# Optimization experiments

Hardware: AMD Instinct MI355X
Metric: run time of the kernel (lower is better)

The kernel has to match this reference:

```python
import jax, jax.numpy as jnp
import numpy as np

N_ENTITIES = 200000
N_USERS = 100000
DIM = 64
N_EDGES = 1000000
N_INTER = 1000000
N_REL = 33
N_INTERACTION_TYPES = 8


def segment_softmax(x, seg, num_segments):
    # two-pass numerically stable segment softmax (torch_scatter.scatter_softmax)
    m = jax.ops.segment_max(x, seg, num_segments=num_segments)
    e = jnp.exp(x - m[seg])
    s = jax.ops.segment_sum(e, seg, num_segments=num_segments)
    return e / s[seg]


def setup_inputs() -> dict:
    key = jax.random.key(0)
    ks = jax.random.split(key, 9)
    return {
        "entity_emb": jax.random.normal(ks[0], (N_ENTITIES, DIM), dtype=jnp.float32),
        "user_emb": jax.random.normal(ks[1], (N_USERS, DIM), dtype=jnp.float32),
        "interaction_emb": jax.random.normal(ks[2], (N_INTERACTION_TYPES, DIM), dtype=jnp.float32),
        "relation_emb": jax.random.normal(ks[3], (N_REL, DIM), dtype=jnp.float32),
        "edge_index": jax.random.randint(ks[4], (2, N_EDGES), 0, N_ENTITIES, dtype=jnp.int32),
        "edge_type": jax.random.randint(ks[5], (N_EDGES,), 1, N_REL, dtype=jnp.int32),
        "user_index": jax.random.randint(ks[6], (N_INTER,), 0, N_USERS, dtype=jnp.int32),
        "item_index": jax.random.randint(ks[7], (N_INTER,), 0, N_ENTITIES, dtype=jnp.int32),
        "interact_type": jax.random.randint(ks[8], (N_INTER,), 0, N_INTERACTION_TYPES, dtype=jnp.int32),
    }


def reference(entity_emb, user_emb, interaction_emb, relation_emb,
              edge_index, edge_type, user_index, item_index, interact_type):
    n_entities = entity_emb.shape[0]
    n_users = user_emb.shape[0]
    head, tail = edge_index[0], edge_index[1]

    # --- entity aggregation over KG edges ---
    neigh = entity_emb[tail]                                      # [E, D]
    w1 = jnp.sum(neigh * relation_emb[edge_type - 1], axis=1) / 8.0   # [E]
    w1 = segment_softmax(w1, head, n_entities)[:, None]           # [E, 1]
    entity_agg = jax.ops.segment_sum(neigh * w1, head, num_segments=n_entities)  # [n_entities, D]

    # --- user aggregation over interactions (agg_method='attention') ---
    interact_entity_emb = entity_emb[item_index]                  # [I, D]
    att = jnp.sum(interaction_emb[interact_type] * user_emb[user_index] * interact_entity_emb, axis=1)  # [I]
    att_w = segment_softmax(att, user_index, n_users)[:, None]    # [I, 1]
    user_agg = jax.ops.segment_sum(att_w * interact_entity_emb, user_index, num_segments=n_users)  # [n_users, D]

    return entity_agg, user_agg, att_w, w1
```

## Files before the change

### kernel.cpp

```cpp
#include <hip/hip_runtime.h>
#include <hip/hip_bf16.h>
#include <hip/hip_fp16.h>

#define DIM 64
#define RELS 32
#define SCAN_B 512
#define TILE_V 64

__device__ __forceinline__ unsigned int pk_h2(float a, float b) {
    __half2 h = __float22half2_rn(make_float2(a, b));
    return *reinterpret_cast<unsigned int*>(&h);
}
__device__ __forceinline__ float4 h4_to_f4(uint2 u) {
    __half2 h0 = *reinterpret_cast<__half2*>(&u.x);
    __half2 h1 = *reinterpret_cast<__half2*>(&u.y);
    float2 f0 = __half22float2(h0);
    float2 f1 = __half22float2(h1);
    return make_float4(f0.x, f0.y, f1.x, f1.y);
}

__global__ __launch_bounds__(256, 4) void buildM_deg(
    const float* __restrict__ ent, const float* __restrict__ rel,
    __hip_bfloat16* __restrict__ M, uint2* __restrict__ entH,
    const int* __restrict__ head, const int* __restrict__ uidx,
    unsigned int* __restrict__ degS,
    unsigned char* __restrict__ rank_e, unsigned char* __restrict__ rank_i,
    int nE, int E, int I, int gM, int Q, int NSEG) {
    __shared__ float4 entL[TILE_V * 17];
    __shared__ float relS[4][16][33];
    int tx = threadIdx.x;
    int bid = blockIdx.x;
    int g = bid / 7, slot = bid - g * 7;

    if (slot >= 2) {
        int t = (g * 5 + (slot - 2)) * 256 + tx;
        if (t < E + I) {
            int k = (t >= Q) + (t >= 2 * Q) + (t >= 3 * Q);
            unsigned int* dk = degS + (size_t)k * NSEG;
            if (t < E) {
                rank_e[t] = (unsigned char)atomicAdd(&dk[head[t]], 1u);
            } else {
                int e = t - E;
                rank_i[e] = (unsigned char)atomicAdd(&dk[nE + uidx[e]], 1u);
            }
        }
        return;
    }

    int mb = g * 2 + slot;
    if (mb >= gM) return;
    int vg = tx >> 4, rg = tx & 15;
    int base = mb * TILE_V;
    const float4* rel4 = (const float4*)rel;
    #pragma unroll
    for (int k = 0; k < 2; k++) {
        int idx = tx + k * 256;
        float4 v = rel4[idx];
        int r = idx >> 4, d4 = idx & 15;
        relS[0][d4][r] = v.x; relS[1][d4][r] = v.y;
        relS[2][d4][r] = v.z; relS[3][d4][r] = v.w;
    }
    const float4* ent4 = (const float4*)ent;
    #pragma unroll
    for (int k = 0; k < 4; k++) {
        int idx = tx + k * 256;
        int row = idx >> 4, col = idx & 15;
        int v = base + row;
        float4 val = make_float4(0.f, 0.f, 0.f, 0.f);
        if (v < nE) {
            val = ent4[(size_t)v * 16 + col];
            entH[(size_t)v * 16 + col] = make_uint2(pk_h2(val.x, val.y), pk_h2(val.z, val.w));
        }
        entL[row * 17 + col] = val;
    }
    __syncthreads();

    float acc[4][2] = {{0.f,0.f},{0.f,0.f},{0.f,0.f},{0.f,0.f}};
    int r0 = rg * 2;
    #pragma unroll 2
    for (int d4 = 0; d4 < 16; d4++) {
        float4 a0 = entL[(vg * 4 + 0) * 17 + d4];
        float4 a1 = entL[(vg * 4 + 1) * 17 + d4];
        float4 a2 = entL[(vg * 4 + 2) * 17 + d4];
        float4 a3 = entL[(vg * 4 + 3) * 17 + d4];
        float bx0 = relS[0][d4][r0],     by0 = relS[1][d4][r0];
        float bz0 = relS[2][d4][r0],     bw0 = relS[3][d4][r0];
        float bx1 = relS[0][d4][r0 + 1], by1 = relS[1][d4][r0 + 1];
        float bz1 = relS[2][d4][r0 + 1], bw1 = relS[3][d4][r0 + 1];
        acc[0][0] = fmaf(a0.x,bx0, fmaf(a0.y,by0, fmaf(a0.z,bz0, fmaf(a0.w,bw0, acc[0][0]))));
        acc[1][0] = fmaf(a1.x,bx0, fmaf(a1.y,by0, fmaf(a1.z,bz0, fmaf(a1.w,bw0, acc[1][0]))));
        acc[2][0] = fmaf(a2.x,bx0, fmaf(a2.y,by0, fmaf(a2.z,bz0, fmaf(a2.w,bw0, acc[2][0]))));
        acc[3][0] = fmaf(a3.x,bx0, fmaf(a3.y,by0, fmaf(a3.z,bz0, fmaf(a3.w,bw0, acc[3][0]))));
        acc[0][1] = fmaf(a0.x,bx1, fmaf(a0.y,by1, fmaf(a0.z,bz1, fmaf(a0.w,bw1, acc[0][1]))));
        acc[1][1] = fmaf(a1.x,bx1, fmaf(a1.y,by1, fmaf(a1.z,bz1, fmaf(a1.w,bw1, acc[1][1]))));
        acc[2][1] = fmaf(a2.x,bx1, fmaf(a2.y,by1, fmaf(a2.z,bz1, fmaf(a2.w,bw1, acc[2][1]))));
        acc[3][1] = fmaf(a3.x,bx1, fmaf(a3.y,by1, fmaf(a3.z,bz1, fmaf(a3.w,bw1, acc[3][1]))));
    }
    __hip_bfloat162* M2 = (__hip_bfloat162*)M;
    #pragma unroll
    for (int i = 0; i < 4; i++) {
        int v = base + vg * 4 + i;
        if (v < nE) {
            __hip_bfloat16 h0 = __float2bfloat16(acc[i][0] * 0.125f);
            __hip_bfloat16 h1 = __float2bfloat16(acc[i][1] * 0.125f);
            M2[(size_t)v * 16 + rg] = __halves2bfloat162(h0, h1);
        }
    }
}

__global__ __launch_bounds__(SCAN_B) void scan_partial(
    const unsigned int* __restrict__ degS, unsigned int* __restrict__ part, int n) {
    __shared__ unsigned int lds[SCAN_B];
    int i = blockIdx.x * SCAN_B + threadIdx.x;
    unsigned int v = 0;
    if (i < n) v = degS[i] + degS[n + i] + degS[2 * (size_t)n + i] + degS[3 * (size_t)n + i];
    lds[threadIdx.x] = v;
    __syncthreads();
    for (int off = SCAN_B >> 1; off > 0; off >>= 1) {
        if (threadIdx.x < off) lds[threadIdx.x] += lds[threadIdx.x + off];
        __syncthreads();
    }
    if (threadIdx.x == 0) part[blockIdx.x] = lds[0];
}

__global__ __launch_bounds__(1024) void scan_block(unsigned int* __restrict__ part, int nb) {
    __shared__ unsigned int lds[1024];
    int t = threadIdx.x;
    unsigned int v = (t < nb) ? part[t] : 0u;
    lds[t] = v;
    __syncthreads();
    for (int off = 1; off < 1024; off <<= 1) {
        unsigned int x = (t >= off) ? lds[t - off] : 0u;
        __syncthreads();
        lds[t] += x;
        __syncthreads();
    }
    if (t < nb) part[t] = lds[t] - v;
}

__global__ __launch_bounds__(SCAN_B) void scan_final(
    const unsigned int* __restrict__ degS, const unsigned int* __restrict__ part,
    unsigned int* __restrict__ offs0, unsigned int* __restrict__ offs123,
    int n, unsigned int total) {
    __shared__ unsigned int lds[SCAN_B];
    int t = threadIdx.x;
    int i = blockIdx.x * SCAN_B + t;
    unsigned int a0 = 0, a1 = 0, a2 = 0, a3 = 0, tot = 0;
    if (i < n) {
        a0 = degS[i]; a1 = degS[n + i];
        a2 = degS[2 * (size_t)n + i]; a3 = degS[3 * (size_t)n + i];
        tot = a0 + a1 + a2 + a3;
    }
    lds[t] = tot;
    __syncthreads();
    for (int off = 1; off < SCAN_B; off <<= 1) {
        unsigned int x = (t >= off) ? lds[t - off] : 0u;
        __syncthreads();
        lds[t] += x;
        __syncthreads();
    }
    if (i < n) {
        unsigned int base = part[blockIdx.x] + lds[t] - tot;
        offs0[i] = base;
        offs123[i] = base + a0;
        offs123[(size_t)n + i] = base + a0 + a1;
        offs123[2 * (size_t)n + i] = base + a0 + a1 + a2;
    }
    if (blockIdx.x == 0 && t == 0) offs0[n] = total;
}

__global__ __launch_bounds__(256) void scatter32(
    const __hip_bfloat16* __restrict__ M,
    const int* __restrict__ head, const int* __restrict__ tail, const int* __restrict__ etype,
    const int* __restrict__ uidx, const int* __restrict__ iidx, const int* __restrict__ ttype,
    const unsigned char* __restrict__ rank_e, const unsigned char* __restrict__ rank_i,
    const unsigned int* __restrict__ offs0, const unsigned int* __restrict__ offs123,
    unsigned long long* __restrict__ pay64, unsigned int* __restrict__ payu,
    float* __restrict__ e_sc, unsigned int* __restrict__ slotu,
    int E, int I, int nE, int Q, int NSEG) {
    int t = blockIdx.x * blockDim.x + threadIdx.x;
    if (t >= E + I) return;
    int k = (t >= Q) + (t >= 2 * Q) + (t >= 3 * Q);
    if (t < E) {
        int s = head[t];
        unsigned int base = (k == 0) ? offs0[s] : offs123[(size_t)(k - 1) * NSEG + s];
        int tl = tail[t];
        float sc = __bfloat162float(M[(size_t)tl * RELS + (etype[t] - 1)]);
        e_sc[t] = sc;
        unsigned int p = base + rank_e[t];
        unsigned long long v = ((unsigned long long)__float_as_uint(sc) << 32) | (unsigned int)tl;
        __builtin_nontemporal_store(v, &pay64[p]);
    } else {
        int e = t - E;
        int s = nE + uidx[e];
        unsigned int base = (k == 0) ? offs0[s] : offs123[(size_t)(k - 1) * NSEG + s];
        unsigned int p = base + rank_i[e] - (unsigned)E;
        unsigned int v = (unsigned int)iidx[e] | ((unsigned int)ttype[e] << 27);
        __builtin_nontemporal_store(v, &payu[p]);
        slotu[e] = p;
    }
}

__global__ __launch_bounds__(256) void fused_agg(
    const uint2* __restrict__ entH, const float* __restrict__ usr,
    const float* __restrict__ itc,
    const unsigned long long* __restrict__ pay64, const unsigned int* __restrict__ payu,
    const unsigned int* __restrict__ offs0,
    float* __restrict__ patt, float2* __restrict__ msum,
    float* __restrict__ aggE, float* __restrict__ aggU,
    int nE, int nU, int E, int gAE) {
    __shared__ float4 itcL[8][16];
    int tx = threadIdx.x;
    int bid = blockIdx.x;

    if (bid < gAE) {
        int t = bid * 256 + tx;
        int h = t >> 4, l = t & 15;
        if (h >= nE) return;
        unsigned int off = offs0[h];
        unsigned int d = offs0[h + 1] - off;
        float m = -3.0e38f, inv = 0.f;
        float4 acc = make_float4(0.f, 0.f, 0.f, 0.f);
        if (d) {
            float m0 = -3.0e38f, s0 = 0.f, m1 = -3.0e38f, s1 = 0.f;
            float4 A0 = make_float4(0.f,0.f,0.f,0.f), A1 = make_float4(0.f,0.f,0.f,0.f);
            unsigned long long v0 = pay64[off];
            uint2 b0 = entH[(size_t)(unsigned int)(v0 & 0xffffffffu) * 16 + l];
            unsigned long long v1 = 0; uint2 b1 = b0;
            if (d > 1) { v1 = pay64[off + 1]; b1 = entH[(size_t)(unsigned int)(v1 & 0xffffffffu) * 16 + l]; }
            for (unsigned int j = 0; j < d; j += 2) {
                unsigned long long nv0 = v0, nv1 = v1; uint2 nb0 = b0, nb1 = b1;
                if (j + 2 < d) { nv0 = pay64[off + j + 2]; nb0 = entH[(size_t)(unsigned int)(nv0 & 0xffffffffu) * 16 + l]; }
                if (j + 3 < d) { nv1 = pay64[off + j + 3]; nb1 = entH[(size_t)(unsigned int)(nv1 & 0xffffffffu) * 16 + l]; }
                {
                    float sc = __uint_as_float((unsigned int)(v0 >> 32));
                    float mn = fmaxf(m0, sc);
                    float sca = __expf(m0 - mn), w = __expf(sc - mn);
                    float4 a = h4_to_f4(b0);
                    s0 = s0 * sca + w;
                    A0.x = A0.x * sca + w * a.x; A0.y = A0.y * sca + w * a.y;
                    A0.z = A0.z * sca + w * a.z; A0.w = A0.w * sca + w * a.w;
                    m0 = mn;
                }
                if (j + 1 < d) {
                    float sc = __uint_as_float((unsigned int)(v1 >> 32));
                    float mn = fmaxf(m1, sc);
                    float sca = __expf(m1 - mn), w = __expf(sc - mn);
                    float4 a = h4_to_f4(b1);
                    s1 = s1 * sca + w;
                    A1.x = A1.x * sca + w * a.x; A1.y = A1.y * sca + w * a.y;
                    A1.z = A1.z * sca + w * a.z; A1.w = A1.w * sca + w * a.w;
                    m1 = mn;
                }
                v0 = nv0; b0 = nb0; v1 = nv1; b1 = nb1;
            }
            float mn = fmaxf(m0, m1);
            float e0 = __expf(m0 - mn), e1 = __expf(m1 - mn);
            float s = s0 * e0 + s1 * e1;
            inv = 1.f / s;
            acc.x = A0.x * e0 + A1.x * e1; acc.y = A0.y * e0 + A1.y * e1;
            acc.z = A0.z * e0 + A1.z * e1; acc.w = A0.w * e0 + A1.w * e1;
            m = mn;
        }
        if (l == 0) msum[h] = make_float2(m, inv);
        acc.x *= inv; acc.y *= inv; acc.z *= inv; acc.w *= inv;
        ((float4*)(aggE + (size_t)h * DIM))[l] = acc;
        return;
    }

    if (tx < 128) itcL[tx >> 4][tx & 15] = ((const float4*)itc)[tx];
    __syncthreads();
    int t = (bid - gAE) * 256 + tx;
    int h = t >> 4, l = t & 15;
    if (h >= nU) return;
    int hs = nE + h;
    unsigned int off = offs0[hs] - (unsigned)E;
    unsigned int d = offs0[hs + 1] - offs0[hs];
    float m = -3.0e38f, inv = 0.f;
    float4 acc = make_float4(0.f, 0.f, 0.f, 0.f);
    float4 ur = ((const float4*)(usr + (size_t)h * DIM))[l];
    if (d) {
        float m0 = -3.0e38f, s0 = 0.f, m1 = -3.0e38f, s1 = 0.f;
        float4 A0 = make_float4(0.f,0.f,0.f,0.f), A1 = make_float4(0.f,0.f,0.f,0.f);
        unsigned int v0 = payu[off];
        uint2 b0 = entH[(size_t)(v0 & 0x7ffffffu) * 16 + l];
        unsigned int v1 = 0; uint2 b1 = b0;
        if (d > 1) { v1 = payu[off + 1]; b1 = entH[(size_t)(v1 & 0x7ffffffu) * 16 + l]; }
        for (unsigned int j = 0; j < d; j += 2) {
            unsigned int nv0 = v0, nv1 = v1; uint2 nb0 = b0, nb1 = b1;
            if (j + 2 < d) { nv0 = payu[off + j + 2]; nb0 = entH[(size_t)(nv0 & 0x7ffffffu) * 16 + l]; }
            if (j + 3 < d) { nv1 = payu[off + j + 3]; nb1 = entH[(size_t)(nv1 & 0x7ffffffu) * 16 + l]; }
            {
                float4 a = h4_to_f4(b0);
                float4 c = itcL[v0 >> 27][l];
                float p = a.x * ur.x * c.x + a.y * ur.y * c.y
                        + a.z * ur.z * c.z + a.w * ur.w * c.w;
                p += __shfl_xor(p, 1);
                p += __shfl_xor(p, 2);
                p += __shfl_xor(p, 4);
                p += __shfl_xor(p, 8);
                if (l == 0) patt[off + j] = p;
                float mn = fmaxf(m0, p);
                float sca = __expf(m0 - mn), w = __expf(p - mn);
                s0 = s0 * sca + w;
                A0.x = A0.x * sca + w * a.x; A0.y = A0.y * sca + w * a.y;
                A0.z = A0.z * sca + w * a.z; A0.w = A0.w * sca + w * a.w;
                m0 = mn;
            }
            if (j + 1 < d) {
                float4 a = h4_to_f4(b1);
                float4 c = itcL[v1 >> 27][l];
                float p = a.x * ur.x * c.x + a.y * ur.y * c.y
                        + a.z * ur.z * c.z + a.w * ur.w * c.w;
                p += __shfl_xor(p, 1);
                p += __shfl_xor(p, 2);
                p += __shfl_xor(p, 4);
                p += __shfl_xor(p, 8);
                if (l == 0) patt[off + j + 1] = p;
                float mn = fmaxf(m1, p);
                float sca = __expf(m1 - mn), w = __expf(p - mn);
                s1 = s1 * sca + w;
                A1.x = A1.x * sca + w * a.x; A1.y = A1.y * sca + w * a.y;
                A1.z = A1.z * sca + w * a.z; A1.w = A1.w * sca + w * a.w;
                m1 = mn;
            }
            v0 = nv0; b0 = nb0; v1 = nv1; b1 = nb1;
        }
        float mn = fmaxf(m0, m1);
        float e0 = __expf(m0 - mn), e1 = __expf(m1 - mn);
        float s = s0 * e0 + s1 * e1;
        inv = 1.f / s;
        acc.x = A0.x * e0 + A1.x * e1; acc.y = A0.y * e0 + A1.y * e1;
        acc.z = A0.z * e0 + A1.z * e1; acc.w = A0.w * e0 + A1.w * e1;
        m = mn;
    }
    if (l == 0) msum[hs] = make_float2(m, inv);
    acc.x *= inv; acc.y *= inv; acc.z *= inv; acc.w *= inv;
    ((float4*)(aggU + (size_t)h * DIM))[l] = acc;
}

__global__ __launch_bounds__(256) void wout(
    const int* __restrict__ head, const int* __restrict__ uidx,
    const float* __restrict__ e_sc, const float* __restrict__ patt,
    const unsigned int* __restrict__ slotu, const float2* __restrict__ msum,
    float* __restrict__ w1, float* __restrict__ attw, int E, int I, int nE) {
    int t = blockIdx.x * blockDim.x + threadIdx.x;
    if (t < E) {
        float2 mi = msum[head[t]];
        w1[t] = __expf(e_sc[t] - mi.x) * mi.y;
    } else if (t < E + I) {
        int e = t - E;
        float2 mi = msum[nE + uidx[e]];
        attw[e] = __expf(patt[slotu[e]] - mi.x) * mi.y;
    }
}

extern "C" void kernel_launch(void* const* d_in, const int* in_sizes, int n_in,
                              void* d_out, int out_size, void* d_ws, size_t ws_size,
                              hipStream_t stream) {
    const float* ent  = (const float*)d_in[0];
    const float* usr  = (const float*)d_in[1];
    const float* itc  = (const float*)d_in[2];
    const float* rel  = (const float*)d_in[3];
    const int* eidx   = (const int*)d_in[4];
    const int* etype  = (const int*)d_in[5];
    const int* uidx   = (const int*)d_in[6];
    const int* iidx   = (const int*)d_in[7];
    const int* ttype  = (const int*)d_in[8];

    const int E  = in_sizes[4] / 2;
    const int I  = in_sizes[6];
    const int nE = in_sizes[0] / DIM;
    const int nU = in_sizes[1] / DIM;
    const int* head = eidx;
    const int* tail = eidx + E;
    const int NSEG = nE + nU;
    const int NB = (NSEG + SCAN_B - 1) / SCAN_B;
    const int Q = (E + I + 3) / 4;

    float* out_entity = (float*)d_out;
    float* out_user   = out_entity + (size_t)nE * DIM;
    float* out_attw   = out_user + (size_t)nU * DIM;
    float* out_w1     = out_attw + I;

    unsigned int* degS      = (unsigned int*)d_ws;
    unsigned int* offs0     = degS + 4 * (size_t)NSEG;
    unsigned int* offs123   = offs0 + NSEG + 2;
    unsigned int* part      = offs123 + 3 * (size_t)NSEG;
    unsigned long long* pay64 = (unsigned long long*)(part + 1024);
    unsigned int* payu      = (unsigned int*)(pay64 + E);
    float* e_sc             = (float*)(payu + I);
    unsigned int* slotu     = (unsigned int*)(e_sc + E);
    unsigned int* Mreg      = slotu + I;
    __hip_bfloat16* M       = (__hip_bfloat16*)Mreg;
    float2* msum            = (float2*)Mreg;
    float* patt             = (float*)(msum + NSEG);
    uint2* entH             = (uint2*)(Mreg + (size_t)nE * 16);
    unsigned char* rank_e   = (unsigned char*)(entH + (size_t)nE * 16);
    unsigned char* rank_i   = rank_e + E;

    hipMemsetAsync(degS, 0, 4 * (size_t)NSEG * sizeof(unsigned int), stream);

    const int T = 256;
    const int gM  = (nE + TILE_V - 1) / TILE_V;
    const int gD  = (E + I + T - 1) / T;
    const int NG  = ((gM + 1) / 2 > (gD + 4) / 5) ? (gM + 1) / 2 : (gD + 4) / 5;
    const int gAE = (int)(((size_t)nE * 16 + T - 1) / T);
    const int gAU = (int)(((size_t)nU * 16 + T - 1) / T);

    buildM_deg<<<dim3((unsigned)(NG * 7)), T, 0, stream>>>(
        ent, rel, M, entH, head, uidx, degS, rank_e, rank_i, nE, E, I, gM, Q, NSEG);

    scan_partial<<<dim3((unsigned)NB), SCAN_B, 0, stream>>>(degS, part, NSEG);
    scan_block<<<dim3(1), 1024, 0, stream>>>(part, NB);
    scan_final<<<dim3((unsigned)NB), SCAN_B, 0, stream>>>(
        degS, part, offs0, offs123, NSEG, (unsigned)(E + I));

    scatter32<<<dim3((unsigned)gD), T, 0, stream>>>(
        M, head, tail, etype, uidx, iidx, ttype, rank_e, rank_i, offs0, offs123,
        pay64, payu, e_sc, slotu, E, I, nE, Q, NSEG);

    fused_agg<<<dim3((unsigned)(gAE + gAU)), T, 0, stream>>>(
        entH, usr, itc, pay64, payu, offs0, patt, msum,
        out_entity, out_user, nE, nU, E, gAE);

    wout<<<dim3((unsigned)gD), T, 0, stream>>>(
        head, uidx, e_sc, patt, slotu, msum, out_w1, out_attw, E, I, nE);
}
```

Baseline: 297.9 us.

## Sort segments by degree to balance aggregation work across wavefronts

Adds a counting sort of entity and user segments by degree (capped at 63), using histogram, scan and scatter kernels, and has fused_agg process segments in that sorted order. Lanes in a wavefront then handle segments of similar length, which cuts the divergence where short segments wait on long ones. The aggregation loop also goes from two interleaved online-softmax streams back to a single stream with one-step prefetch. The cost is five extra small launches, indirect writes to scattered output rows, and less memory-level parallelism per segment.

```diff
diff --git a/kernel.cpp b/kernel.cpp
--- a/kernel.cpp
+++ b/kernel.cpp
@@ -167,6 +167,62 @@
         offs123[2 * (size_t)n + i] = base + a0 + a1 + a2;
     }
     if (blockIdx.x == 0 && t == 0) offs0[n] = total;
+}
+
+__global__ __launch_bounds__(256) void sort_hist(
+    const unsigned int* __restrict__ offs0, unsigned int* __restrict__ bins,
+    int lo, int n) {
+    __shared__ unsigned int h[64];
+    int tx = threadIdx.x;
+    if (tx < 64) h[tx] = 0;
+    __syncthreads();
+    int i = blockIdx.x * 256 + tx;
+    if (i < n) {
+        int s = lo + i;
+        unsigned int d = offs0[s + 1] - offs0[s];
+        atomicAdd(&h[d < 63u ? d : 63u], 1u);
+    }
+    __syncthreads();
+    if (tx < 64 && h[tx]) atomicAdd(&bins[tx], h[tx]);
+}
+
+__global__ __launch_bounds__(128) void sort_scan(unsigned int* __restrict__ bins, int nE) {
+    __shared__ unsigned int lds[128];
+    int t = threadIdx.x;
+    int half = t >> 6;
+    unsigned int v = bins[t];
+    lds[t] = v;
+    __syncthreads();
+    for (int off = 1; off < 64; off <<= 1) {
+        unsigned int x = 0;
+        if ((t & 63) >= off) x = lds[t - off];
+        __syncthreads();
+        lds[t] += x;
+        __syncthreads();
+    }
+    bins[t] = (half ? (unsigned)nE : 0u) + lds[t] - v;
+}
+
+__global__ __launch_bounds__(256) void sort_scatter(
+    const unsigned int* __restrict__ offs0, unsigned int* __restrict__ cursor,
+    unsigned int* __restrict__ order, int lo, int n, int binBase) {
+    __shared__ unsigned int lh[64], lbase[64];
+    int tx = threadIdx.x;
+    if (tx < 64) lh[tx] = 0;
+    __syncthreads();
+    int i = blockIdx.x * 256 + tx;
+    unsigned int b = 0, r = 0;
+    bool act = (i < n);
+    int s = lo + i;
+    if (act) {
+        unsigned int d = offs0[s + 1] - offs0[s];
+        b = d < 63u ? d : 63u;
+        r = atomicAdd(&lh[b], 1u);
+    }
+    __syncthreads();
+    if (tx < 64 && lh[tx]) lbase[tx] = atomicAdd(&cursor[binBase + tx], lh[tx]);
+    __syncthreads();
+    if (act) order[lbase[b] + r] = (unsigned int)s;
 }
 
 __global__ __launch_bounds__(256) void scatter32(
@@ -205,7 +261,7 @@
     const uint2* __restrict__ entH, const float* __restrict__ usr,
     const float* __restrict__ itc,
     const unsigned long long* __restrict__ pay64, const unsigned int* __restrict__ payu,
-    const unsigned int* __restrict__ offs0,
+    const unsigned int* __restrict__ offs0, const unsigned int* __restrict__ order,
     float* __restrict__ patt, float2* __restrict__ msum,
     float* __restrict__ aggE, float* __restrict__ aggU,
     int nE, int nU, int E, int gAE) {
@@ -215,52 +271,35 @@
 
     if (bid < gAE) {
         int t = bid * 256 + tx;
-        int h = t >> 4, l = t & 15;
-        if (h >= nE) return;
+        int slot = t >> 4, l = t & 15;
+        if (slot >= nE) return;
+        int h = (int)order[slot];
         unsigned int off = offs0[h];
         unsigned int d = offs0[h + 1] - off;
-        float m = -3.0e38f, inv = 0.f;
+        float m = -3.0e38f, s = 0.f, inv = 0.f;
         float4 acc = make_float4(0.f, 0.f, 0.f, 0.f);
         if (d) {
-            float m0 = -3.0e38f, s0 = 0.f, m1 = -3.0e38f, s1 = 0.f;
-            float4 A0 = make_float4(0.f,0.f,0.f,0.f), A1 = make_float4(0.f,0.f,0.f,0.f);
             unsigned long long v0 = pay64[off];
             uint2 b0 = entH[(size_t)(unsigned int)(v0 & 0xffffffffu) * 16 + l];
-            unsigned long long v1 = 0; uint2 b1 = b0;
-            if (d > 1) { v1 = pay64[off + 1]; b1 = entH[(size_t)(unsigned int)(v1 & 0xffffffffu) * 16 + l]; }
-            for (unsigned int j = 0; j < d; j += 2) {
-                unsigned long long nv0 = v0, nv1 = v1; uint2 nb0 = b0, nb1 = b1;
-                if (j + 2 < d) { nv0 = pay64[off + j + 2]; nb0 = entH[(size_t)(unsigned int)(nv0 & 0xffffffffu) * 16 + l]; }
-                if (j + 3 < d) { nv1 = pay64[off + j + 3]; nb1 = entH[(size_t)(unsigned int)(nv1 & 0xffffffffu) * 16 + l]; }
-                {
-                    float sc = __uint_as_float((unsigned int)(v0 >> 32));
-                    float mn = fmaxf(m0, sc);
-                    float sca = __expf(m0 - mn), w = __expf(sc - mn);
-                    float4 a = h4_to_f4(b0);
-                    s0 = s0 * sca + w;
-                    A0.x = A0.x * sca + w * a.x; A0.y = A0.y * sca + w * a.y;
-                    A0.z = A0.z * sca + w * a.z; A0.w = A0.w * sca + w * a.w;
-                    m0 = mn;
+            for (unsigned int j = 0; j < d; j++) {
+                unsigned long long v1 = v0; uint2 b1 = b0;
+                if (j + 1 < d) {
+                    v1 = pay64[off + j + 1];
+                    b1 = entH[(size_t)(unsigned int)(v1 & 0xffffffffu) * 16 + l];
                 }
-                if (j + 1 < d) {
-                    float sc = __uint_as_float((unsigned int)(v1 >> 32));
-                    float mn = fmaxf(m1, sc);
-                    float sca = __expf(m1 - mn), w = __expf(sc - mn);
-                    float4 a = h4_to_f4(b1);
-                    s1 = s1 * sca + w;
-                    A1.x = A1.x * sca + w * a.x; A1.y = A1.y * sca + w * a.y;
-                    A1.z = A1.z * sca + w * a.z; A1.w = A1.w * sca + w * a.w;
-                    m1 = mn;
-                }
-                v0 = nv0; b0 = nb0; v1 = nv1; b1 = nb1;
+                float sc = __uint_as_float((unsigned int)(v0 >> 32));
+                float4 a0 = h4_to_f4(b0);
+                float mn = fmaxf(m, sc);
+                float scale = __expf(m - mn);
+                float w = __expf(sc - mn);
+                s = s * scale + w;
+                acc.x = acc.x * scale + w * a0.x;
+                acc.y = acc.y * scale + w * a0.y;
+                acc.z = acc.z * scale + w * a0.z;
+                acc.w = acc.w * scale + w * a0.w;
+                m = mn; v0 = v1; b0 = b1;
             }
-            float mn = fmaxf(m0, m1);
-            float e0 = __expf(m0 - mn), e1 = __expf(m1 - mn);
-            float s = s0 * e0 + s1 * e1;
             inv = 1.f / s;
-            acc.x = A0.x * e0 + A1.x * e1; acc.y = A0.y * e0 + A1.y * e1;
-            acc.z = A0.z * e0 + A1.z * e1; acc.w = A0.w * e0 + A1.w * e1;
-            m = mn;
         }
         if (l == 0) msum[h] = make_float2(m, inv);
         acc.x *= inv; acc.y *= inv; acc.z *= inv; acc.w *= inv;
@@ -271,68 +310,44 @@
     if (tx < 128) itcL[tx >> 4][tx & 15] = ((const float4*)itc)[tx];
     __syncthreads();
     int t = (bid - gAE) * 256 + tx;
-    int h = t >> 4, l = t & 15;
-    if (h >= nU) return;
-    int hs = nE + h;
+    int slot = t >> 4, l = t & 15;
+    if (slot >= nU) return;
+    int hs = (int)order[nE + slot];
+    int h = hs - nE;
     unsigned int off = offs0[hs] - (unsigned)E;
     unsigned int d = offs0[hs + 1] - offs0[hs];
-    float m = -3.0e38f, inv = 0.f;
+    float m = -3.0e38f, s = 0.f, inv = 0.f;
     float4 acc = make_float4(0.f, 0.f, 0.f, 0.f);
     float4 ur = ((const float4*)(usr + (size_t)h * DIM))[l];
     if (d) {
-        float m0 = -3.0e38f, s0 = 0.f, m1 = -3.0e38f, s1 = 0.f;
-        float4 A0 = make_float4(0.f,0.f,0.f,0.f), A1 = make_float4(0.f,0.f,0.f,0.f);
         unsigned int v0 = payu[off];
         uint2 b0 = entH[(size_t)(v0 & 0x7ffffffu) * 16 + l];
-        unsigned int v1 = 0; uint2 b1 = b0;
-        if (d > 1) { v1 = payu[off + 1]; b1 = entH[(size_t)(v1 & 0x7ffffffu) * 16 + l]; }
-        for (unsigned int j = 0; j < d; j += 2) {
-            unsigned int nv0 = v0, nv1 = v1; uint2 nb0 = b0, nb1 = b1;
-            if (j + 2 < d) { nv0 = payu[off + j + 2]; nb0 = entH[(size_t)(nv0 & 0x7ffffffu) * 16 + l]; }
-            if (j + 3 < d) { nv1 = payu[off + j + 3]; nb1 = entH[(size_t)(nv1 & 0x7ffffffu) * 16 + l]; }
-            {
-                float4 a = h4_to_f4(b0);
-                float4 c = itcL[v0 >> 27][l];
-                float p = a.x * ur.x * c.x + a.y * ur.y * c.y
-                        + a.z * ur.z * c.z + a.w * ur.w * c.w;
-                p += __shfl_xor(p, 1);
-                p += __shfl_xor(p, 2);
-                p += __shfl_xor(p, 4);
-                p += __shfl_xor(p, 8);
-                if (l == 0) patt[off + j] = p;
-                float mn = fmaxf(m0, p);
-                float sca = __expf(m0 - mn), w = __expf(p - mn);
-                s0 = s0 * sca + w;
-                A0.x = A0.x * sca + w * a.x; A0.y = A0.y * sca + w * a.y;
-                A0.z = A0.z * sca + w * a.z; A0.w = A0.w * sca + w * a.w;
-                m0 = mn;
+        for (unsigned int j = 0; j < d; j++) {
+            unsigned int v1 = v0; uint2 b1 = b0;
+            if (j + 1 < d) {
+                v1 = payu[off + j + 1];
+                b1 = entH[(size_t)(v1 & 0x7ffffffu) * 16 + l];
             }
-            if (j + 1 < d) {
-                float4 a = h4_to_f4(b1);
-                float4 c = itcL[v1 >> 27][l];
-                float p = a.x * ur.x * c.x + a.y * ur.y * c.y
-                        + a.z * ur.z * c.z + a.w * ur.w * c.w;
-                p += __shfl_xor(p, 1);
-                p += __shfl_xor(p, 2);
-                p += __shfl_xor(p, 4);
-                p += __shfl_xor(p, 8);
-                if (l == 0) patt[off + j + 1] = p;
-                float mn = fmaxf(m1, p);
-                float sca = __expf(m1 - mn), w = __expf(p - mn);
-                s1 = s1 * sca + w;
-                A1.x = A1.x * sca + w * a.x; A1.y = A1.y * sca + w * a.y;
-                A1.z = A1.z * sca + w * a.z; A1.w = A1.w * sca + w * a.w;
-                m1 = mn;
-            }
-            v0 = nv0; b0 = nb0; v1 = nv1; b1 = nb1;
+            float4 a0 = h4_to_f4(b0);
+            float4 c = itcL[v0 >> 27][l];
+            float p = a0.x * ur.x * c.x + a0.y * ur.y * c.y
+                    + a0.z * ur.z * c.z + a0.w * ur.w * c.w;
+            p += __shfl_xor(p, 1);
+            p += __shfl_xor(p, 2);
+            p += __shfl_xor(p, 4);
+            p += __shfl_xor(p, 8);
+            if (l == 0) patt[off + j] = p;
+            float mn = fmaxf(m, p);
+            float scale = __expf(m - mn);
+            float w = __expf(p - mn);
+            s = s * scale + w;
+            acc.x = acc.x * scale + w * a0.x;
+            acc.y = acc.y * scale + w * a0.y;
+            acc.z = acc.z * scale + w * a0.z;
+            acc.w = acc.w * scale + w * a0.w;
+            m = mn; v0 = v1; b0 = b1;
         }
-        float mn = fmaxf(m0, m1);
-        float e0 = __expf(m0 - mn), e1 = __expf(m1 - mn);
-        float s = s0 * e0 + s1 * e1;
         inv = 1.f / s;
-        acc.x = A0.x * e0 + A1.x * e1; acc.y = A0.y * e0 + A1.y * e1;
-        acc.z = A0.z * e0 + A1.z * e1; acc.w = A0.w * e0 + A1.w * e1;
-        m = mn;
     }
     if (l == 0) msum[hs] = make_float2(m, inv);
     acc.x *= inv; acc.y *= inv; acc.z *= inv; acc.w *= inv;
@@ -384,10 +399,14 @@
     float* out_w1     = out_attw + I;
 
     unsigned int* degS      = (unsigned int*)d_ws;
-    unsigned int* offs0     = degS + 4 * (size_t)NSEG;
+    unsigned int* sortb     = degS + 4 * (size_t)NSEG;
+    unsigned int* offs0     = sortb + 128;
     unsigned int* offs123   = offs0 + NSEG + 2;
     unsigned int* part      = offs123 + 3 * (size_t)NSEG;
-    unsigned long long* pay64 = (unsigned long long*)(part + 1024);
+    unsigned int* order     = part + 1024;
+    unsigned int* padw      = order + NSEG;
+    unsigned long long* pay64 = (unsigned long long*)(((size_t)(padw - (unsigned int*)d_ws) & 1)
+                                ? padw + 1 : padw);
     unsigned int* payu      = (unsigned int*)(pay64 + E);
     float* e_sc             = (float*)(payu + I);
     unsigned int* slotu     = (unsigned int*)(e_sc + E);
@@ -399,7 +418,7 @@
     unsigned char* rank_e   = (unsigned char*)(entH + (size_t)nE * 16);
     unsigned char* rank_i   = rank_e + E;
 
-    hipMemsetAsync(degS, 0, 4 * (size_t)NSEG * sizeof(unsigned int), stream);
+    hipMemsetAsync(degS, 0, (4 * (size_t)NSEG + 128) * sizeof(unsigned int), stream);
 
     const int T = 256;
     const int gM  = (nE + TILE_V - 1) / TILE_V;
@@ -407,6 +426,8 @@
     const int NG  = ((gM + 1) / 2 > (gD + 4) / 5) ? (gM + 1) / 2 : (gD + 4) / 5;
     const int gAE = (int)(((size_t)nE * 16 + T - 1) / T);
     const int gAU = (int)(((size_t)nU * 16 + T - 1) / T);
+    const int gSE = (nE + T - 1) / T;
+    const int gSU = (nU + T - 1) / T;
 
     buildM_deg<<<dim3((unsigned)(NG * 7)), T, 0, stream>>>(
         ent, rel, M, entH, head, uidx, degS, rank_e, rank_i, nE, E, I, gM, Q, NSEG);
@@ -416,12 +437,18 @@
     scan_final<<<dim3((unsigned)NB), SCAN_B, 0, stream>>>(
         degS, part, offs0, offs123, NSEG, (unsigned)(E + I));
 
+    sort_hist<<<dim3((unsigned)gSE), T, 0, stream>>>(offs0, sortb, 0, nE);
+    sort_hist<<<dim3((unsigned)gSU), T, 0, stream>>>(offs0, sortb + 64, nE, nU);
+    sort_scan<<<dim3(1), 128, 0, stream>>>(sortb, nE);
+    sort_scatter<<<dim3((unsigned)gSE), T, 0, stream>>>(offs0, sortb, order, 0, nE, 0);
+    sort_scatter<<<dim3((unsigned)gSU), T, 0, stream>>>(offs0, sortb, order, nE, nU, 64);
+
     scatter32<<<dim3((unsigned)gD), T, 0, stream>>>(
         M, head, tail, etype, uidx, iidx, ttype, rank_e, rank_i, offs0, offs123,
         pay64, payu, e_sc, slotu, E, I, nE, Q, NSEG);
 
     fused_agg<<<dim3((unsigned)(gAE + gAU)), T, 0, stream>>>(
-        entH, usr, itc, pay64, payu, offs0, patt, msum,
+        entH, usr, itc, pay64, payu, offs0, order, patt, msum,
         out_entity, out_user, nE, nU, E, gAE);
 
     wout<<<dim3((unsigned)gD), T, 0, stream>>>(
```

After: 338.1 us. +13.5%, slower.
